# Kernel tuning notes

Hardware: AMD Instinct MI355X
Metric: run time of the kernel (lower is better)

Reference implementation:

```python
import jax, jax.numpy as jnp
import numpy as np

N_NODES = 50000
N_EDGES = 800000
D = 128
LN_EPS = 1e-5


def setup_inputs() -> dict:
    key = jax.random.key(0)
    ks = jax.random.split(key, 6)
    x = jax.random.normal(ks[0], (N_NODES, D), dtype=jnp.float32)
    edge_index = jax.random.randint(ks[1], (2, N_EDGES), 0, N_NODES, dtype=jnp.int32)
    # MeanAggregator.linear: (D -> D)
    agg_W = jax.random.normal(ks[2], (D, D), dtype=jnp.float32) / np.sqrt(D)
    agg_b = jnp.zeros((D,), dtype=jnp.float32)
    # GraphSAGELayer.linear: (2D -> D)
    W = jax.random.normal(ks[3], (2 * D, D), dtype=jnp.float32) / np.sqrt(2 * D)
    b = jnp.zeros((D,), dtype=jnp.float32)
    gamma = jnp.ones((D,), dtype=jnp.float32)
    beta = jnp.zeros((D,), dtype=jnp.float32)
    return {"x": x, "edge_index": edge_index, "agg_W": agg_W, "agg_b": agg_b,
            "W": W, "b": b, "gamma": gamma, "beta": beta}


def reference(x, edge_index, agg_W, agg_b, W, b, gamma, beta):
    row, col = edge_index[0], edge_index[1]
    num_nodes = x.shape[0]
    # mean aggregation: scatter-add source features x[row] into destination col
    nbr_sum = jax.ops.segment_sum(x[row], col, num_segments=num_nodes)  # [N, D]
    deg = jax.ops.segment_sum(jnp.ones_like(col, dtype=x.dtype), col,
                              num_segments=num_nodes)
    deg = jnp.clip(deg, 1.0)
    aggregated = nbr_sum / deg[:, None]
    agg_features = aggregated @ agg_W + agg_b  # MeanAggregator.linear
    combined = jnp.concatenate([x, agg_features], axis=-1)  # [N, 2D]
    out = jax.nn.relu(combined @ W + b)
    # LayerNorm over last dim
    mu = jnp.mean(out, axis=-1, keepdims=True)
    var = jnp.var(out, axis=-1, keepdims=True)
    out = (out - mu) * jax.lax.rsqrt(var + LN_EPS) * gamma + beta
    # dropout: inference mode -> identity
    return out
```

## Files before the change

### kernel.cpp

```cpp
#include <hip/hip_runtime.h>

#define N_NODES 50000
#define N_EDGES 800000
#define D_FEAT 128
#define LN_EPS 1e-5f
#define TM 128
#define CVT_B 3125
#define NBUCK 391
#define BCAP 3072
#define BIN1_E 4096
#define BIN1_B 196

typedef __attribute__((ext_vector_type(8))) short bf16x8;
typedef __attribute__((ext_vector_type(4))) float f32x4;

__device__ __forceinline__ unsigned short f2bf(float f) {
    union { float f; unsigned int i; } v; v.f = f;
    unsigned int x = v.i;
    unsigned int lsb = (x >> 16) & 1u;
    x += 0x7fffu + lsb;
    return (unsigned short)(x >> 16);
}
__device__ __forceinline__ float bflo(unsigned int u) {
    union { unsigned int i; float f; } v; v.i = u << 16; return v.f;
}
__device__ __forceinline__ float bfhi(unsigned int u) {
    union { unsigned int i; float f; } v; v.i = u & 0xffff0000u; return v.f;
}
__device__ __forceinline__ int clampn(int v) {
    return (v < 0) ? 0 : ((v >= N_NODES) ? (N_NODES - 1) : v);
}
__device__ __forceinline__ void split2(float f0, float f1,
                                       unsigned int& hp, unsigned int& lp) {
    unsigned short h0 = f2bf(f0), h1 = f2bf(f1);
    unsigned short l0 = f2bf(f0 - bflo(h0)), l1 = f2bf(f1 - bflo(h1));
    hp = ((unsigned)h1 << 16) | h0;
    lp = ((unsigned)l1 << 16) | l0;
}

__global__ __launch_bounds__(256) void prep_kernel(
        const float* __restrict__ x,
        const int* __restrict__ ei,
        const float* __restrict__ agg_W,
        const float* __restrict__ agg_b,
        const float* __restrict__ W,
        const float* __restrict__ b,
        uint4* __restrict__ AH4,
        uint4* __restrict__ AL4,
        unsigned int* __restrict__ bcurs,
        unsigned int* __restrict__ binned,
        unsigned short* __restrict__ Wt2h,
        unsigned short* __restrict__ Wt2l,
        float* __restrict__ cvec)
{
    __shared__ int esrc[BIN1_E];
    __shared__ unsigned short edst[BIN1_E];
    __shared__ int hist[NBUCK];
    __shared__ unsigned int cur2[NBUCK];

    int blk = blockIdx.x;
    if (blk < CVT_B) {
        int i = blk * 256 + threadIdx.x;
        const float4 a = *(const float4*)(x + (size_t)i * 8);
        const float4 c = *(const float4*)(x + (size_t)i * 8 + 4);
        uint4 h, l;
        split2(a.x, a.y, h.x, l.x);
        split2(a.z, a.w, h.y, l.y);
        split2(c.x, c.y, h.z, l.z);
        split2(c.z, c.w, h.w, l.w);
        size_t idx = (size_t)(i >> 4) * 32 + (i & 15);
        AH4[idx] = h;
        AL4[idx] = l;
    } else if (blk < CVT_B + BIN1_B) {
        int t    = threadIdx.x;
        int base = (blk - CVT_B) * BIN1_E;

        for (int i = t; i < NBUCK; i += 256) hist[i] = 0;
        #pragma unroll
        for (int i = 0; i < BIN1_E / 256; ++i) {
            int idx = i * 256 + t;
            int e = base + idx;
            if (e < N_EDGES) {
                esrc[idx] = clampn(ei[e]);
                edst[idx] = (unsigned short)clampn(ei[N_EDGES + e]);
            } else {
                esrc[idx] = -1;
            }
        }
        __syncthreads();

        #pragma unroll
        for (int i = 0; i < BIN1_E / 256; ++i) {
            int idx = i * 256 + t;
            if (esrc[idx] >= 0) atomicAdd(&hist[(int)edst[idx] >> 7], 1);
        }
        __syncthreads();

        for (int bk = t; bk < NBUCK; bk += 256) {
            int c = hist[bk];
            unsigned int off = c ? atomicAdd(&bcurs[bk], (unsigned int)c) : 0u;
            cur2[bk] = (unsigned int)bk * BCAP + off;
        }
        __syncthreads();

        #pragma unroll
        for (int i = 0; i < BIN1_E / 256; ++i) {
            int idx = i * 256 + t;
            int src = esrc[idx];
            if (src >= 0) {
                int dst = (int)edst[idx];
                int bk  = dst >> 7;
                unsigned int slot = atomicAdd(&cur2[bk], 1u);
                if (slot < (unsigned int)bk * BCAP + BCAP)
                    binned[slot] = (unsigned int)src | ((unsigned int)dst << 16);
            }
        }
    } else {
        int t = blk - CVT_B - BIN1_B;
        int n = threadIdx.x;
        if (n < 128) {
            float w1 = W[t * 128 + n];
            unsigned short h1 = f2bf(w1);
            Wt2h[n * 256 + t] = h1;
            Wt2l[n * 256 + t] = f2bf(w1 - bflo(h1));
            float m = 0.0f;
            for (int j = 0; j < 128; ++j)
                m += agg_W[t * 128 + j] * W[(128 + j) * 128 + n];
            unsigned short h2 = f2bf(m);
            Wt2h[n * 256 + 128 + t] = h2;
            Wt2l[n * 256 + 128 + t] = f2bf(m - bflo(h2));
            if (t == 0) {
                float s = b[n];
                for (int j = 0; j < 128; ++j)
                    s += agg_b[j] * W[(128 + j) * 128 + n];
                cvec[n] = s;
            }
        }
    }
}

__global__ __launch_bounds__(512) void binpass2_kernel(const unsigned int* __restrict__ binned,
                                                       const unsigned int* __restrict__ bcurs,
                                                       int* __restrict__ pos,
                                                       int* __restrict__ deg_cnt,
                                                       unsigned short* __restrict__ edge_src)
{
    __shared__ int lscan[128];
    __shared__ int lcnt[128];
    __shared__ int lcur[128];
    int bk = blockIdx.x, t = threadIdx.x;

    unsigned int cnt = bcurs[bk]; if (cnt > BCAP) cnt = BCAP;
    unsigned int start = (unsigned int)bk * BCAP;
    unsigned int end   = start + cnt;

    int n0 = bk << 7;
    int nn = N_NODES - n0; if (nn > 128) nn = 128;

    if (t < 128) lcnt[t] = 0;
    __syncthreads();
    for (unsigned int e = start + t; e < end; e += 512)
        atomicAdd(&lcnt[(int)(binned[e] >> 16) & 127], 1);
    __syncthreads();

    int lv = (t < 128) ? lcnt[t] : 0;
    if (t < 128) lscan[t] = lv;
    __syncthreads();
    for (int off = 1; off < 128; off <<= 1) {
        int u = (t >= off && t < 128) ? lscan[t - off] : 0;
        __syncthreads();
        if (t < 128) lscan[t] += u;
        __syncthreads();
    }
    if (t < 128) {
        int ls = (int)start + lscan[t] - lv;
        lcur[t] = ls;
        if (t < nn) {
            pos[n0 + t]     = ls + lv;
            deg_cnt[n0 + t] = lv;
        }
    }
    __syncthreads();

    for (unsigned int e = start + t; e < end; e += 512) {
        unsigned int v = binned[e];
        int slot = atomicAdd(&lcur[(int)(v >> 16) & 127], 1);
        edge_src[slot] = (unsigned short)(v & 0xffffu);
    }
}

__global__ void gather_kernel(uint4* __restrict__ AH4,
                              uint4* __restrict__ AL4,
                              const int* __restrict__ pos,
                              const int* __restrict__ deg_cnt,
                              const unsigned short* __restrict__ edge_src)
{
    int tid  = threadIdx.x;
    int node = blockIdx.x * 4 + (tid >> 6);
    int lane = tid & 63;
    int quarter = lane >> 4;
    int sub     = lane & 15;
    if (node >= N_NODES) return;

    int end   = pos[node];
    int dcnt  = deg_cnt[node];
    int start = end - dcnt;

    float a0 = 0.f, a1 = 0.f, a2 = 0.f, a3 = 0.f,
          a4 = 0.f, a5 = 0.f, a6 = 0.f, a7 = 0.f;

    for (int b = start; b < end; b += 64) {
        int nb = end - b; if (nb > 64) nb = 64;
        int sid = (b + lane < end) ? (int)edge_src[b + lane] : 0;
        for (int j = 0; j < nb; j += 4) {
            int eidx = j + quarter;
            int s = __shfl(sid, eidx, 64);
            if (eidx < nb) {
                const uint4 v = AH4[(size_t)s * 32 + sub];
                a0 += bflo(v.x); a1 += bfhi(v.x);
                a2 += bflo(v.y); a3 += bfhi(v.y);
                a4 += bflo(v.z); a5 += bfhi(v.z);
                a6 += bflo(v.w); a7 += bfhi(v.w);
            }
        }
    }
    #pragma unroll
    for (int m = 16; m <= 32; m <<= 1) {
        a0 += __shfl_xor(a0, m, 64); a1 += __shfl_xor(a1, m, 64);
        a2 += __shfl_xor(a2, m, 64); a3 += __shfl_xor(a3, m, 64);
        a4 += __shfl_xor(a4, m, 64); a5 += __shfl_xor(a5, m, 64);
        a6 += __shfl_xor(a6, m, 64); a7 += __shfl_xor(a7, m, 64);
    }
    if (quarter == 0) {
        float inv = 1.0f / (float)((dcnt > 1) ? dcnt : 1);
        uint4 h, l;
        split2(a0 * inv, a1 * inv, h.x, l.x);
        split2(a2 * inv, a3 * inv, h.y, l.y);
        split2(a4 * inv, a5 * inv, h.z, l.z);
        split2(a6 * inv, a7 * inv, h.w, l.w);
        size_t idx = (size_t)node * 32 + 16 + sub;
        AH4[idx] = h;
        AL4[idx] = l;
    }
}

__global__ __launch_bounds__(256) void gsage_main(
        const unsigned short* __restrict__ AH,
        const unsigned short* __restrict__ AL,
        const unsigned short* __restrict__ Wt2h,
        const unsigned short* __restrict__ Wt2l,
        const float* __restrict__ cvec,
        const float* __restrict__ gamma,
        const float* __restrict__ beta,
        float* __restrict__ out)
{
    int tid  = threadIdx.x;
    int lane = tid & 63;
    int w    = tid >> 6;
    int l15  = lane & 15, grp = lane >> 4;
    int node0 = blockIdx.x * TM;

    f32x4 acc[2][8];
    #pragma unroll
    for (int m = 0; m < 2; ++m)
        #pragma unroll
        for (int nf = 0; nf < 8; ++nf)
            acc[m][nf] = (f32x4){0.f, 0.f, 0.f, 0.f};

    int row0 = node0 + w * 32 + l15;
    int rA0 = (row0      < N_NODES) ? row0      : (N_NODES - 1);
    int rA1 = (row0 + 16 < N_NODES) ? row0 + 16 : (N_NODES - 1);
    const unsigned short* pAH0 = AH + (size_t)rA0 * 256;
    const unsigned short* pAL0 = AL + (size_t)rA0 * 256;
    const unsigned short* pAH1 = AH + (size_t)rA1 * 256;
    const unsigned short* pAL1 = AL + (size_t)rA1 * 256;
    const unsigned short* pB   = Wt2h + (size_t)l15 * 256;
    const unsigned short* pBl  = Wt2l + (size_t)l15 * 256;

    #pragma unroll
    for (int c = 0; c < 4; ++c) {
        #pragma unroll
        for (int ks = 0; ks < 2; ++ks) {
            int krel = c * 64 + ks * 32 + grp * 8;

            bf16x8 ah0 = *(const bf16x8*)(pAH0 + krel);
            bf16x8 al0 = *(const bf16x8*)(pAL0 + krel);
            bf16x8 ah1 = *(const bf16x8*)(pAH1 + krel);
            bf16x8 al1 = *(const bf16x8*)(pAL1 + krel);

            #pragma unroll
            for (int nf = 0; nf < 8; ++nf) {
                bf16x8 bh = *(const bf16x8*)(pB  + (size_t)nf * 16 * 256 + krel);
                bf16x8 bl = *(const bf16x8*)(pBl + (size_t)nf * 16 * 256 + krel);
                acc[0][nf] = __builtin_amdgcn_mfma_f32_16x16x32_bf16(ah0, bh, acc[0][nf], 0, 0, 0);
                acc[0][nf] = __builtin_amdgcn_mfma_f32_16x16x32_bf16(al0, bh, acc[0][nf], 0, 0, 0);
                acc[0][nf] = __builtin_amdgcn_mfma_f32_16x16x32_bf16(ah0, bl, acc[0][nf], 0, 0, 0);
                acc[1][nf] = __builtin_amdgcn_mfma_f32_16x16x32_bf16(ah1, bh, acc[1][nf], 0, 0, 0);
                acc[1][nf] = __builtin_amdgcn_mfma_f32_16x16x32_bf16(al1, bh, acc[1][nf], 0, 0, 0);
                acc[1][nf] = __builtin_amdgcn_mfma_f32_16x16x32_bf16(ah1, bl, acc[1][nf], 0, 0, 0);
            }
        }
    }

    float cv[8], gv[8], bv[8];
    #pragma unroll
    for (int nf = 0; nf < 8; ++nf) {
        int col = nf * 16 + l15;
        cv[nf] = cvec[col]; gv[nf] = gamma[col]; bv[nf] = beta[col];
    }

    #pragma unroll
    for (int m = 0; m < 2; ++m) {
        #pragma unroll
        for (int r = 0; r < 4; ++r) {
            float s1 = 0.f, s2 = 0.f;
            #pragma unroll
            for (int nf = 0; nf < 8; ++nf) {
                float v = acc[m][nf][r] + cv[nf];
                v = (v > 0.f) ? v : 0.f;
                acc[m][nf][r] = v;
                s1 += v; s2 += v * v;
            }
            #pragma unroll
            for (int msk = 1; msk < 16; msk <<= 1) {
                s1 += __shfl_xor(s1, msk, 64);
                s2 += __shfl_xor(s2, msk, 64);
            }
            float mu   = s1 * (1.0f / 128.0f);
            float var  = s2 * (1.0f / 128.0f) - mu * mu;
            float rstd = rsqrtf(var + LN_EPS);
            int node = node0 + w * 32 + m * 16 + grp * 4 + r;
            if (node < N_NODES) {
                #pragma unroll
                for (int nf = 0; nf < 8; ++nf)
                    out[(size_t)node * D_FEAT + nf * 16 + l15] =
                        (acc[m][nf][r] - mu) * rstd * gv[nf] + bv[nf];
            }
        }
    }
}

extern "C" void kernel_launch(void* const* d_in, const int* in_sizes, int n_in,
                              void* d_out, int out_size, void* d_ws, size_t ws_size,
                              hipStream_t stream) {
    const float* x     = (const float*)d_in[0];
    const int*   ei    = (const int*)d_in[1];
    const float* agg_W = (const float*)d_in[2];
    const float* agg_b = (const float*)d_in[3];
    const float* W     = (const float*)d_in[4];
    const float* b     = (const float*)d_in[5];
    const float* gamma = (const float*)d_in[6];
    const float* beta  = (const float*)d_in[7];
    float*       out   = (float*)d_out;

    size_t out_bytes = (size_t)out_size * sizeof(float);

    if (n_in != 8)                       { hipMemsetAsync(d_out, 0x45, out_bytes, stream); return; }
    if (in_sizes[0] != N_NODES * D_FEAT) { hipMemsetAsync(d_out, 0x48, out_bytes, stream); return; }
    if (in_sizes[1] != 2 * N_EDGES)      { hipMemsetAsync(d_out, 0x49, out_bytes, stream); return; }
    if (out_size != N_NODES * D_FEAT)    { hipMemsetAsync(d_out, 0x47, out_bytes, stream); return; }

    int*   deg_cnt  = (int*)d_ws;
    int*   pos      = deg_cnt + N_NODES;
    unsigned short* edge_src = (unsigned short*)(pos + N_NODES);
    unsigned short* Wt2h = (unsigned short*)((int*)edge_src + N_EDGES);
    unsigned short* Wt2l = Wt2h + 128 * 256;
    float* cvec     = (float*)(Wt2l + 128 * 256);
    unsigned short* AH = (unsigned short*)(cvec + 128);
    unsigned short* AL = AH + (size_t)N_NODES * 256;
    size_t need_ws = ((size_t)N_NODES * 2 + N_EDGES + 256 * 128 + 128) * 4
                     + (size_t)N_NODES * 256 * 2 * 2;
    if (ws_size < need_ws)               { hipMemsetAsync(d_out, 0x46, out_bytes, stream); return; }

    unsigned int* binned = (unsigned int*)d_out;
    unsigned int* bcurs  = binned + (size_t)NBUCK * BCAP;

    hipMemsetAsync(bcurs, 0, NBUCK * sizeof(unsigned int), stream);
    prep_kernel<<<CVT_B + BIN1_B + 128, 256, 0, stream>>>(
        x, ei, agg_W, agg_b, W, b, (uint4*)AH, (uint4*)AL, bcurs, binned,
        Wt2h, Wt2l, cvec);
    binpass2_kernel<<<NBUCK, 512, 0, stream>>>(binned, bcurs, pos, deg_cnt, edge_src);
    gather_kernel<<<(N_NODES + 3) / 4, 256, 0, stream>>>(
        (uint4*)AH, (uint4*)AL, pos, deg_cnt, edge_src);
    gsage_main<<<(N_NODES + TM - 1) / TM, 256, 0, stream>>>(
        AH, AL, Wt2h, Wt2l, cvec, gamma, beta, out);
}
```

Before: 191.1 us.

## Stage weight tiles in padded LDS with register prefetch in main GEMM

```diff
diff --git a/kernel.cpp b/kernel.cpp
--- a/kernel.cpp
+++ b/kernel.cpp
@@ -254,11 +254,27 @@
         const float* __restrict__ beta,
         float* __restrict__ out)
 {
+    __shared__ unsigned short Bh[128][72];
+    __shared__ unsigned short Bl[128][72];
+
     int tid  = threadIdx.x;
     int lane = tid & 63;
     int w    = tid >> 6;
     int l15  = lane & 15, grp = lane >> 4;
     int node0 = blockIdx.x * TM;
+
+    int scol  = tid >> 1;
+    int spart = tid & 1;
+    const uint4* srcH = (const uint4*)Wt2h + scol * 32 + spart * 4;
+    const uint4* srcL = (const uint4*)Wt2l + scol * 32 + spart * 4;
+    uint4* dstH = (uint4*)&Bh[scol][spart * 32];
+    uint4* dstL = (uint4*)&Bl[scol][spart * 32];
+
+    uint4 rH[4], rL[4];
+    #pragma unroll
+    for (int j = 0; j < 4; ++j) { rH[j] = srcH[j]; rL[j] = srcL[j]; }
+    #pragma unroll
+    for (int j = 0; j < 4; ++j) { dstH[j] = rH[j]; dstL[j] = rL[j]; }
 
     f32x4 acc[2][8];
     #pragma unroll
@@ -274,11 +290,18 @@
     const unsigned short* pAL0 = AL + (size_t)rA0 * 256;
     const unsigned short* pAH1 = AH + (size_t)rA1 * 256;
     const unsigned short* pAL1 = AL + (size_t)rA1 * 256;
-    const unsigned short* pB   = Wt2h + (size_t)l15 * 256;
-    const unsigned short* pBl  = Wt2l + (size_t)l15 * 256;
-
-    #pragma unroll
+
+    __syncthreads();
+
     for (int c = 0; c < 4; ++c) {
+        if (c < 3) {
+            #pragma unroll
+            for (int j = 0; j < 4; ++j) {
+                rH[j] = srcH[(c + 1) * 8 + j];
+                rL[j] = srcL[(c + 1) * 8 + j];
+            }
+        }
+
         #pragma unroll
         for (int ks = 0; ks < 2; ++ks) {
             int krel = c * 64 + ks * 32 + grp * 8;
@@ -290,8 +313,9 @@
 
             #pragma unroll
             for (int nf = 0; nf < 8; ++nf) {
-                bf16x8 bh = *(const bf16x8*)(pB  + (size_t)nf * 16 * 256 + krel);
-                bf16x8 bl = *(const bf16x8*)(pBl + (size_t)nf * 16 * 256 + krel);
+                int col = nf * 16 + l15;
+                bf16x8 bh = *(const bf16x8*)&Bh[col][ks * 32 + grp * 8];
+                bf16x8 bl = *(const bf16x8*)&Bl[col][ks * 32 + grp * 8];
                 acc[0][nf] = __builtin_amdgcn_mfma_f32_16x16x32_bf16(ah0, bh, acc[0][nf], 0, 0, 0);
                 acc[0][nf] = __builtin_amdgcn_mfma_f32_16x16x32_bf16(al0, bh, acc[0][nf], 0, 0, 0);
                 acc[0][nf] = __builtin_amdgcn_mfma_f32_16x16x32_bf16(ah0, bl, acc[0][nf], 0, 0, 0);
@@ -299,6 +323,13 @@
                 acc[1][nf] = __builtin_amdgcn_mfma_f32_16x16x32_bf16(al1, bh, acc[1][nf], 0, 0, 0);
                 acc[1][nf] = __builtin_amdgcn_mfma_f32_16x16x32_bf16(ah1, bl, acc[1][nf], 0, 0, 0);
             }
+        }
+
+        if (c < 3) {
+            __syncthreads();
+            #pragma unroll
+            for (int j = 0; j < 4; ++j) { dstH[j] = rH[j]; dstL[j] = rL[j]; }
+            __syncthreads();
         }
     }
 
```

After: 189.9 us. About the same (-0.6%).
